# Performance work log

Measured on AMD Instinct MI355X. Metric: run time of the kernel, lower is better.

## Reference

```python
import jax, jax.numpy as jnp
import numpy as np

B, N, K = 4096, 16384, 512

def setup_inputs() -> dict:
    key = jax.random.key(0)
    x = jax.random.normal(key, (B, N), dtype=jnp.float32)
    return {"x": x, "k": K}

def reference(x, k):
    # top-k of |x| along dim 1 (last dim for 2D x)
    _, top_idxs = jax.lax.top_k(jnp.abs(x), k)          # [B, k]
    rows = jnp.arange(x.shape[0])[:, None]               # [B, 1]
    mask = jnp.zeros(x.shape, dtype=bool).at[rows, top_idxs].set(True)
    return x * mask
```

## Files before the change

kernel.cpp:

```cpp
#include <hip/hip_runtime.h>

#define TPB 1024
#define NW (TPB / 64)
#define NCOLS 16384
#define F4PT 4
#define NELEM 16
#define BINS1 8192
#define SH1 18
#define CAP 1024

__device__ __forceinline__ unsigned keyOf(float f) {
    return __float_as_uint(f) & 0x7fffffffu;
}

template <int NBINS>
__device__ void suffix_select(const unsigned* hist, unsigned Krem,
                              unsigned* wsums, unsigned* bc) {
    const int t = threadIdx.x;
    const int lane = t & 63;
    const int wave = t >> 6;
    constexpr int CH = (NBINS + TPB - 1) / TPB;
    const int base = t * CH;
    unsigned c = 0;
#pragma unroll
    for (int i = 0; i < CH; ++i)
        if (base + i < NBINS) c += hist[base + i];
    unsigned s = c;
#pragma unroll
    for (int off = 1; off < 64; off <<= 1) {
        unsigned o = __shfl_down(s, off);
        if (lane + off < 64) s += o;
    }
    if (lane == 0) wsums[wave] = s;
    __syncthreads();
    if (wave == 0) {
        unsigned ws = (lane < NW) ? wsums[lane] : 0u;
        unsigned ss = ws;
#pragma unroll
        for (int off = 1; off < 64; off <<= 1) {
            unsigned o = __shfl_down(ss, off);
            if (lane + off < 64) ss += o;
        }
        if (lane < NW) wsums[lane] = ss;
    }
    __syncthreads();
    unsigned gts = ((wave + 1 < NW) ? wsums[wave + 1] : 0u) + (s - c);
    if (gts < Krem && gts + c >= Krem) {
        unsigned cum = gts;
        for (int i = CH - 1; i >= 0; --i) {
            unsigned h = hist[base + i];
            cum += h;
            if (cum >= Krem) {
                bc[0] = (unsigned)(base + i);
                bc[1] = Krem - (cum - h);
                bc[2] = h;
                break;
            }
        }
    }
    __syncthreads();
}

__global__ __launch_bounds__(TPB, 8) void topk_mask_kernel(
        const float* __restrict__ x, const int* __restrict__ kp,
        float* __restrict__ out) {
    __shared__ unsigned hist[BINS1];
    __shared__ unsigned candKey[CAP];
    __shared__ unsigned candIdx[CAP];
    __shared__ unsigned bitmap[NCOLS / 32];
    __shared__ unsigned wsums[NW];
    __shared__ unsigned bc[3];
    __shared__ unsigned cnt;

    const int t = threadIdx.x;
    const unsigned K = (unsigned)(*kp);
    const size_t row = blockIdx.x;
    const float4* xr = reinterpret_cast<const float4*>(x) + row * (NCOLS / 4);
    float4* orow = reinterpret_cast<float4*>(out) + row * (NCOLS / 4);

    float vals[NELEM];
#pragma unroll
    for (int i = 0; i < F4PT; ++i) {
        float4 tmp = xr[t + i * TPB];
        vals[4 * i + 0] = tmp.x;
        vals[4 * i + 1] = tmp.y;
        vals[4 * i + 2] = tmp.z;
        vals[4 * i + 3] = tmp.w;
    }

#pragma unroll
    for (int i = 0; i < BINS1 / TPB; ++i) hist[t + i * TPB] = 0u;
    if (t < NCOLS / 32) bitmap[t] = 0u;
    if (t == 0) cnt = 0u;
    __syncthreads();

#pragma unroll
    for (int e = 0; e < NELEM; ++e)
        atomicAdd(&hist[keyOf(vals[e]) >> SH1], 1u);
    __syncthreads();
    suffix_select<BINS1>(hist, K, wsums, bc);
    const unsigned cut1 = bc[0];
    const unsigned r1 = bc[1];
    const unsigned E = bc[2];

    unsigned thrKey = 0;
    const bool fastp = (E <= CAP);

    if (fastp) {
#pragma unroll
        for (int e = 0; e < NELEM; ++e) {
            unsigned key = keyOf(vals[e]);
            if ((key >> SH1) == cut1) {
                unsigned idx = 4u * (unsigned)(t + (e >> 2) * TPB) + (e & 3);
                unsigned p = atomicAdd(&cnt, 1u);
                candKey[p] = key;
                candIdx[p] = idx;
            }
        }
        __syncthreads();
        for (unsigned p = t; p < E; p += TPB) {
            unsigned key = candKey[p], idx = candIdx[p], rank = 0;
            for (unsigned q = 0; q < E; ++q) {
                unsigned ck = candKey[q];
                rank += (ck > key) || (ck == key && candIdx[q] < idx);
            }
            if (rank < r1) atomicOr(&bitmap[idx >> 5], 1u << (idx & 31));
        }
        __syncthreads();
    } else {
        if (t < 1024) hist[t] = 0u;
        __syncthreads();
#pragma unroll
        for (int e = 0; e < NELEM; ++e) {
            unsigned key = keyOf(vals[e]);
            if ((key >> SH1) == cut1) atomicAdd(&hist[(key >> 8) & 1023u], 1u);
        }
        __syncthreads();
        suffix_select<1024>(hist, r1, wsums, bc);
        const unsigned pfx = (cut1 << 10) | bc[0];
        const unsigned r2 = bc[1];
        if (t < 256) hist[t] = 0u;
        __syncthreads();
#pragma unroll
        for (int e = 0; e < NELEM; ++e) {
            unsigned key = keyOf(vals[e]);
            if ((key >> 8) == pfx) atomicAdd(&hist[key & 255u], 1u);
        }
        __syncthreads();
        suffix_select<256>(hist, r2, wsums, bc);
        thrKey = (pfx << 8) | bc[0];
        const unsigned rQ = bc[1];
        if (t == 0) cnt = 0u;
        __syncthreads();
#pragma unroll
        for (int e = 0; e < NELEM; ++e) {
            if (keyOf(vals[e]) == thrKey) {
                unsigned idx = 4u * (unsigned)(t + (e >> 2) * TPB) + (e & 3);
                unsigned p = atomicAdd(&cnt, 1u);
                if (p < CAP) candIdx[p] = idx;
            }
        }
        __syncthreads();
        unsigned m = cnt < CAP ? cnt : CAP;
        for (unsigned p = t; p < m; p += TPB) {
            unsigned idx = candIdx[p], rank = 0;
            for (unsigned q = 0; q < m; ++q) rank += candIdx[q] < idx;
            if (rank < rQ) atomicOr(&bitmap[idx >> 5], 1u << (idx & 31));
        }
        __syncthreads();
    }

#pragma unroll
    for (int i = 0; i < F4PT; ++i) {
        float4 o;
#pragma unroll
        for (int j = 0; j < 4; ++j) {
            float v = vals[4 * i + j];
            unsigned key = keyOf(v);
            unsigned idx = 4u * (unsigned)(t + i * TPB) + j;
            bool keep;
            if (fastp) {
                unsigned b = key >> SH1;
                keep = (b > cut1) ||
                       (b == cut1 && ((bitmap[idx >> 5] >> (idx & 31)) & 1u));
            } else {
                keep = (key > thrKey) ||
                       (key == thrKey && ((bitmap[idx >> 5] >> (idx & 31)) & 1u));
            }
            (&o.x)[j] = keep ? v : 0.0f;
        }
        orow[t + i * TPB] = o;
    }
}

extern "C" void kernel_launch(void* const* d_in, const int* in_sizes, int n_in,
                              void* d_out, int out_size, void* d_ws, size_t ws_size,
                              hipStream_t stream) {
    const float* x = (const float*)d_in[0];
    const int* kp = (const int*)d_in[1];
    float* out = (float*)d_out;
    const int rows = in_sizes[0] / NCOLS;
    topk_mask_kernel<<<rows, TPB, 0, stream>>>(x, kp, out);
}
```

Baseline: 153.8 us.

## Halve block size, pad histogram, and pack candidate key+index into one word

Switches to 512 threads per block, each holding 32 elements, and changes the launch bounds. The first-level histogram is padded every 16 bins to spread LDS bank conflicts. Candidates now pack the low key bits with an inverted index into one 32-bit word, so ranking does a single compare per pair instead of two arrays and a tiebreak. It also halves the candidate capacity to 512 and adds an asm barrier to keep values in registers; the smaller capacity sends more rows to the slower three-pass fallback when the boundary bin is large.

```diff
diff --git a/kernel.cpp b/kernel.cpp
--- a/kernel.cpp
+++ b/kernel.cpp
@@ -1,19 +1,21 @@
 #include <hip/hip_runtime.h>
 
-#define TPB 1024
+#define TPB 512
 #define NW (TPB / 64)
 #define NCOLS 16384
-#define F4PT 4
-#define NELEM 16
+#define F4PT 8
+#define EPT 32
 #define BINS1 8192
 #define SH1 18
-#define CAP 1024
+#define HSZ (BINS1 + BINS1 / 16)
+#define CAP 512
 
 __device__ __forceinline__ unsigned keyOf(float f) {
     return __float_as_uint(f) & 0x7fffffffu;
 }
-
-template <int NBINS>
+__device__ __forceinline__ unsigned padded(unsigned b) { return b + (b >> 4); }
+
+template <int NBINS, bool PAD>
 __device__ void suffix_select(const unsigned* hist, unsigned Krem,
                               unsigned* wsums, unsigned* bc) {
     const int t = threadIdx.x;
@@ -23,8 +25,10 @@
     const int base = t * CH;
     unsigned c = 0;
 #pragma unroll
-    for (int i = 0; i < CH; ++i)
-        if (base + i < NBINS) c += hist[base + i];
+    for (int i = 0; i < CH; ++i) {
+        int b = base + i;
+        if (b < NBINS) c += hist[PAD ? padded((unsigned)b) : (unsigned)b];
+    }
     unsigned s = c;
 #pragma unroll
     for (int off = 1; off < 64; off <<= 1) {
@@ -48,10 +52,12 @@
     if (gts < Krem && gts + c >= Krem) {
         unsigned cum = gts;
         for (int i = CH - 1; i >= 0; --i) {
-            unsigned h = hist[base + i];
+            int b = base + i;
+            if (b >= NBINS) continue;
+            unsigned h = hist[PAD ? padded((unsigned)b) : (unsigned)b];
             cum += h;
             if (cum >= Krem) {
-                bc[0] = (unsigned)(base + i);
+                bc[0] = (unsigned)b;
                 bc[1] = Krem - (cum - h);
                 bc[2] = h;
                 break;
@@ -61,12 +67,11 @@
     __syncthreads();
 }
 
-__global__ __launch_bounds__(TPB, 8) void topk_mask_kernel(
+__global__ __launch_bounds__(TPB, 6) void topk_mask_kernel(
         const float* __restrict__ x, const int* __restrict__ kp,
         float* __restrict__ out) {
-    __shared__ unsigned hist[BINS1];
-    __shared__ unsigned candKey[CAP];
-    __shared__ unsigned candIdx[CAP];
+    __shared__ unsigned hist[HSZ];
+    __shared__ unsigned cand[CAP];
     __shared__ unsigned bitmap[NCOLS / 32];
     __shared__ unsigned wsums[NW];
     __shared__ unsigned bc[3];
@@ -78,7 +83,7 @@
     const float4* xr = reinterpret_cast<const float4*>(x) + row * (NCOLS / 4);
     float4* orow = reinterpret_cast<float4*>(out) + row * (NCOLS / 4);
 
-    float vals[NELEM];
+    float vals[EPT];
 #pragma unroll
     for (int i = 0; i < F4PT; ++i) {
         float4 tmp = xr[t + i * TPB];
@@ -87,18 +92,21 @@
         vals[4 * i + 2] = tmp.z;
         vals[4 * i + 3] = tmp.w;
     }
-
-#pragma unroll
-    for (int i = 0; i < BINS1 / TPB; ++i) hist[t + i * TPB] = 0u;
+#pragma unroll
+    for (int e = 0; e < EPT; ++e) asm volatile("" : "+v"(vals[e]));
+
+#pragma unroll
+    for (int i = 0; i < (HSZ + TPB - 1) / TPB; ++i)
+        if (t + i * TPB < HSZ) hist[t + i * TPB] = 0u;
     if (t < NCOLS / 32) bitmap[t] = 0u;
     if (t == 0) cnt = 0u;
     __syncthreads();
 
 #pragma unroll
-    for (int e = 0; e < NELEM; ++e)
-        atomicAdd(&hist[keyOf(vals[e]) >> SH1], 1u);
-    __syncthreads();
-    suffix_select<BINS1>(hist, K, wsums, bc);
+    for (int e = 0; e < EPT; ++e)
+        atomicAdd(&hist[padded(keyOf(vals[e]) >> SH1)], 1u);
+    __syncthreads();
+    suffix_select<BINS1, true>(hist, K, wsums, bc);
     const unsigned cut1 = bc[0];
     const unsigned r1 = bc[1];
     const unsigned E = bc[2];
@@ -108,63 +116,62 @@
 
     if (fastp) {
 #pragma unroll
-        for (int e = 0; e < NELEM; ++e) {
+        for (int e = 0; e < EPT; ++e) {
             unsigned key = keyOf(vals[e]);
             if ((key >> SH1) == cut1) {
                 unsigned idx = 4u * (unsigned)(t + (e >> 2) * TPB) + (e & 3);
                 unsigned p = atomicAdd(&cnt, 1u);
-                candKey[p] = key;
-                candIdx[p] = idx;
+                cand[p] = ((key & 0x3FFFFu) << 14) | (idx ^ 0x3FFFu);
             }
         }
         __syncthreads();
         for (unsigned p = t; p < E; p += TPB) {
-            unsigned key = candKey[p], idx = candIdx[p], rank = 0;
-            for (unsigned q = 0; q < E; ++q) {
-                unsigned ck = candKey[q];
-                rank += (ck > key) || (ck == key && candIdx[q] < idx);
-            }
-            if (rank < r1) atomicOr(&bitmap[idx >> 5], 1u << (idx & 31));
+            unsigned w = cand[p], rank = 0;
+            for (unsigned q = 0; q < E; ++q) rank += (cand[q] > w);
+            if (rank < r1) {
+                unsigned idx = (w & 0x3FFFu) ^ 0x3FFFu;
+                atomicOr(&bitmap[idx >> 5], 1u << (idx & 31));
+            }
         }
         __syncthreads();
     } else {
         if (t < 1024) hist[t] = 0u;
         __syncthreads();
 #pragma unroll
-        for (int e = 0; e < NELEM; ++e) {
+        for (int e = 0; e < EPT; ++e) {
             unsigned key = keyOf(vals[e]);
             if ((key >> SH1) == cut1) atomicAdd(&hist[(key >> 8) & 1023u], 1u);
         }
         __syncthreads();
-        suffix_select<1024>(hist, r1, wsums, bc);
+        suffix_select<1024, false>(hist, r1, wsums, bc);
         const unsigned pfx = (cut1 << 10) | bc[0];
         const unsigned r2 = bc[1];
         if (t < 256) hist[t] = 0u;
         __syncthreads();
 #pragma unroll
-        for (int e = 0; e < NELEM; ++e) {
+        for (int e = 0; e < EPT; ++e) {
             unsigned key = keyOf(vals[e]);
             if ((key >> 8) == pfx) atomicAdd(&hist[key & 255u], 1u);
         }
         __syncthreads();
-        suffix_select<256>(hist, r2, wsums, bc);
+        suffix_select<256, false>(hist, r2, wsums, bc);
         thrKey = (pfx << 8) | bc[0];
         const unsigned rQ = bc[1];
         if (t == 0) cnt = 0u;
         __syncthreads();
 #pragma unroll
-        for (int e = 0; e < NELEM; ++e) {
+        for (int e = 0; e < EPT; ++e) {
             if (keyOf(vals[e]) == thrKey) {
                 unsigned idx = 4u * (unsigned)(t + (e >> 2) * TPB) + (e & 3);
                 unsigned p = atomicAdd(&cnt, 1u);
-                if (p < CAP) candIdx[p] = idx;
+                if (p < CAP) cand[p] = idx;
             }
         }
         __syncthreads();
         unsigned m = cnt < CAP ? cnt : CAP;
         for (unsigned p = t; p < m; p += TPB) {
-            unsigned idx = candIdx[p], rank = 0;
-            for (unsigned q = 0; q < m; ++q) rank += candIdx[q] < idx;
+            unsigned idx = cand[p], rank = 0;
+            for (unsigned q = 0; q < m; ++q) rank += cand[q] < idx;
             if (rank < rQ) atomicOr(&bitmap[idx >> 5], 1u << (idx & 31));
         }
         __syncthreads();
```

After: 150.5 us. 2.1% less time.
